# Kernel optimization log

Hardware: AMD Instinct MI355X
Metric: run time of the kernel (lower is better)

Reference implementation:

```python
import jax, jax.numpy as jnp
import numpy as np


def setup_inputs() -> dict:
    key = jax.random.key(0)
    k1, k2, k3 = jax.random.split(key, 3)
    B, L, D = 4, 2056, 1024  # L = K + T = 8 + 2048
    x = jax.random.normal(k1, (B, L, D), dtype=jnp.float32)
    # Linear weights stored as (in_features, out_features); no bias (config.bias=False)
    W_attn = jax.random.normal(k2, (D, 3 * D), dtype=jnp.float32) * 0.02
    W_proj = jax.random.normal(k3, (D, D), dtype=jnp.float32) * 0.02
    return {"x": x, "W_attn": W_attn, "W_proj": W_proj, "n_head": 16, "n_memory": 8}


def reference(x, W_attn, W_proj, n_head, n_memory):
    B, L, C = x.shape
    K = n_memory
    T = L - K
    hd = C // n_head
    scale = 1.0 / np.sqrt(hd).astype(np.float32)

    qkv = x @ W_attn                      # (B, L, 3C)
    q, k, v = jnp.split(qkv, 3, axis=2)
    # (B, H, L, hd)
    q = q.reshape(B, L, n_head, hd).transpose(0, 2, 1, 3)
    k = k.reshape(B, L, n_head, hd).transpose(0, 2, 1, 3)
    v = v.reshape(B, L, n_head, hd).transpose(0, 2, 1, 3)

    att = jnp.einsum("bhqd,bhkd->bhqk", q, k) * scale  # (B, H, L, L)

    # Mask: all-True except the (seq x seq) block which is causal (lower-tri).
    # Memory rows (first K) attend everywhere; seq rows attend to all memory + causal seq.
    mask = jnp.ones((L, L), dtype=bool)
    seq_causal = jnp.tril(jnp.ones((T, T), dtype=bool))
    mask = mask.at[K:, K:].set(seq_causal)

    att = jnp.where(mask[None, None, :, :], att, jnp.float32(-jnp.inf))
    att = jax.nn.softmax(att, axis=-1)

    y = jnp.einsum("bhqk,bhkd->bhqd", att, v)  # (B, H, L, hd)
    y = y.transpose(0, 2, 1, 3).reshape(B, L, C)
    return y @ W_proj
```

## Files before the change

### kernel.cpp

```cpp
#include <hip/hip_runtime.h>
#include <hip/hip_bf16.h>
#include <hip/hip_fp16.h>

typedef _Float16 f16x8 __attribute__((ext_vector_type(8)));
typedef _Float16 f16x4 __attribute__((ext_vector_type(4)));
typedef float f32x4 __attribute__((ext_vector_type(4)));

typedef const __attribute__((address_space(1))) void gvoid_t;
typedef __attribute__((address_space(3))) void svoid_t;

constexpr int Bb = 4, Lq = 2056, Dd = 1024, NH = 16, HD = 64, NMEM = 8;
constexpr int Mtot = Bb * Lq;
constexpr int KEYS = 64;
constexpr int NT = (Lq + KEYS - 1) / KEYS;

__device__ inline float fexp2(float x) {
  float r;
  asm("v_exp_f32 %0, %1" : "=v"(r) : "v"(x));
  return r;
}

__global__ __launch_bounds__(256) void cast_f16(const float* __restrict__ in,
                                                _Float16* __restrict__ out, int n8) {
  int i = blockIdx.x * blockDim.x + threadIdx.x;
  if (i >= n8) return;
  const float4* p = reinterpret_cast<const float4*>(in) + (size_t)i * 2;
  float4 a = p[0], b = p[1];
  f16x8 o;
  o[0] = (_Float16)a.x; o[1] = (_Float16)a.y; o[2] = (_Float16)a.z; o[3] = (_Float16)a.w;
  o[4] = (_Float16)b.x; o[5] = (_Float16)b.y; o[6] = (_Float16)b.z; o[7] = (_Float16)b.w;
  *(reinterpret_cast<f16x8*>(out) + i) = o;
}

__global__ void transpose_cast(const float* __restrict__ in, _Float16* __restrict__ out,
                               int rows, int cols) {
  __shared__ float t[32][33];
  int c0 = blockIdx.x * 32, r0 = blockIdx.y * 32;
  int tx = threadIdx.x, ty = threadIdx.y;
#pragma unroll
  for (int i = 0; i < 4; ++i)
    t[ty + i * 8][tx] = in[(size_t)(r0 + ty + i * 8) * cols + c0 + tx];
  __syncthreads();
#pragma unroll
  for (int i = 0; i < 4; ++i)
    out[(size_t)(c0 + ty + i * 8) * rows + r0 + tx] = (_Float16)t[tx][ty + i * 8];
}

template <int EPI>
__global__ __launch_bounds__(256) void gemm_f16(
    const _Float16* __restrict__ A, const _Float16* __restrict__ Bt,
    int M, int N, int Kd, float* __restrict__ Cf,
    _Float16* __restrict__ qout, _Float16* __restrict__ kout, _Float16* __restrict__ vtout) {
  constexpr int BM = 128, BN = 128, BK = 64;
  __shared__ _Float16 smem[2 * BM * BK];
  const int tid = threadIdx.x;
  const int wid = tid >> 6, lane = tid & 63;
  const int wr = wid >> 1, wc = wid & 1;
  const int l16 = lane & 15, lq = lane >> 4;

  const int gx = gridDim.x;
  const int nwg = gx * gridDim.y;
  const int i0 = blockIdx.y * gx + blockIdx.x;
  const int cpx = nwg >> 3;
  const int logical = (i0 & 7) * cpx + (i0 >> 3);
  const int m0 = (logical / gx) * BM, n0 = (logical % gx) * BN;

  f32x4 acc[4][4];
#pragma unroll
  for (int i = 0; i < 4; ++i)
#pragma unroll
    for (int j = 0; j < 4; ++j) acc[i][j] = (f32x4){0.f, 0.f, 0.f, 0.f};

  const int KT = Kd / BK;
  for (int kt = 0; kt < KT; ++kt) {
    const size_t kbase = (size_t)kt * BK;
#pragma unroll
    for (int c = 0; c < 4; ++c) {
      int q = wid * 256 + c * 64 + lane;
      int r = q >> 3, cc = q & 7;
      int gr = m0 + r; gr = gr < M ? gr : M - 1;
      const _Float16* src = A + (size_t)gr * Kd + kbase + ((cc ^ (r & 7)) << 3);
      __builtin_amdgcn_global_load_lds((gvoid_t*)src,
          (svoid_t*)(smem + (size_t)(wid * 256 + c * 64) * 8), 16, 0, 0);
    }
#pragma unroll
    for (int c = 0; c < 4; ++c) {
      int q = wid * 256 + c * 64 + lane;
      int r = q >> 3, cc = q & 7;
      const _Float16* src = Bt + (size_t)(n0 + r) * Kd + kbase + ((cc ^ (r & 7)) << 3);
      __builtin_amdgcn_global_load_lds((gvoid_t*)src,
          (svoid_t*)(smem + BM * BK + (size_t)(wid * 256 + c * 64) * 8), 16, 0, 0);
    }
    __syncthreads();
#pragma unroll
    for (int kk = 0; kk < 2; ++kk) {
      f16x8 af[4], bfr[4];
#pragma unroll
      for (int i = 0; i < 4; ++i) {
        int r = wr * 64 + i * 16 + l16;
        int off = r * 64 + (((kk * 4 + lq) ^ (r & 7)) << 3);
        af[i] = *(const f16x8*)(smem + off);
      }
#pragma unroll
      for (int j = 0; j < 4; ++j) {
        int r = wc * 64 + j * 16 + l16;
        int off = BM * BK + r * 64 + (((kk * 4 + lq) ^ (r & 7)) << 3);
        bfr[j] = *(const f16x8*)(smem + off);
      }
#pragma unroll
      for (int i = 0; i < 4; ++i)
#pragma unroll
        for (int j = 0; j < 4; ++j)
          acc[i][j] = __builtin_amdgcn_mfma_f32_16x16x32_f16(af[i], bfr[j], acc[i][j], 0, 0, 0);
    }
    __syncthreads();
  }

  if (EPI == 1 && n0 >= 2 * Dd) {
#pragma unroll
    for (int i = 0; i < 4; ++i) {
      int mb = m0 + wr * 64 + i * 16 + lq * 4;
      if (mb >= M) continue;
      int b = mb / Lq, l = mb - b * Lq;
#pragma unroll
      for (int j = 0; j < 4; ++j) {
        int n = n0 + wc * 64 + j * 16 + l16;
        int h = (n >> 6) & 15, d = n & 63;
        if (l + 4 <= Lq) {
          f16x4 pk;
          pk[0] = (_Float16)acc[i][j][0]; pk[1] = (_Float16)acc[i][j][1];
          pk[2] = (_Float16)acc[i][j][2]; pk[3] = (_Float16)acc[i][j][3];
          *(f16x4*)(vtout + ((size_t)(b * NH + h) * HD + d) * Lq + l) = pk;
        } else {
#pragma unroll
          for (int r = 0; r < 4; ++r) {
            int m = mb + r;
            if (m >= M) continue;
            int b2 = m / Lq, l2 = m - b2 * Lq;
            vtout[((size_t)(b2 * NH + h) * HD + d) * Lq + l2] = (_Float16)acc[i][j][r];
          }
        }
      }
    }
  } else {
#pragma unroll
    for (int i = 0; i < 4; ++i) {
#pragma unroll
      for (int r = 0; r < 4; ++r) {
        int m = m0 + wr * 64 + i * 16 + lq * 4 + r;
        if (m >= M) continue;
        if (EPI == 0) {
#pragma unroll
          for (int j = 0; j < 4; ++j) {
            int n = n0 + wc * 64 + j * 16 + l16;
            Cf[(size_t)m * N + n] = acc[i][j][r];
          }
        } else {
          int b = m / Lq, l = m - b * Lq;
#pragma unroll
          for (int j = 0; j < 4; ++j) {
            int n = n0 + wc * 64 + j * 16 + l16;
            int which = n >> 10, h = (n >> 6) & 15, d = n & 63;
            int bh = b * NH + h;
            _Float16 v = (_Float16)acc[i][j][r];
            if (which == 0)
              qout[((size_t)bh * Lq + l) * HD + d] = v;
            else
              kout[((size_t)bh * Lq + l) * HD + d] = v;
          }
        }
      }
    }
  }
}

__global__ __launch_bounds__(256) void attn_f16(const _Float16* __restrict__ qm,
                                                const _Float16* __restrict__ km,
                                                const _Float16* __restrict__ vt,
                                                _Float16* __restrict__ y) {
  __shared__ _Float16 kvs[2][2][KEYS * HD];
  __shared__ _Float16 plds[4][16][40];

  const int i0 = blockIdx.y * (int)gridDim.x + blockIdx.x;
  const int logical = (i0 & 7) * (NT * Bb * NH / 8) + (i0 >> 3);
  const int bh = logical / NT;
  const int qtl = logical % NT;
  const int qt = (qtl == 0) ? 0 : (NT - qtl);

  const int wid = threadIdx.x >> 6, lane = threadIdx.x & 63;
  const int l16 = lane & 15, lq = lane >> 4;
  const int qr0 = qt * 64 + wid * 16;

  const _Float16* qbase = qm + (size_t)bh * Lq * HD;
  const _Float16* kbase = km + (size_t)bh * Lq * HD;
  const _Float16* vbase = vt + (size_t)bh * HD * Lq;

  int qrow = qr0 + l16; if (qrow > Lq - 1) qrow = Lq - 1;
  f16x8 qf0 = *(const f16x8*)(qbase + (size_t)qrow * HD + lq * 8);
  f16x8 qf1 = *(const f16x8*)(qbase + (size_t)qrow * HD + 32 + lq * 8);
  const _Float16 QSC = (_Float16)(0.125f * 1.44269504f);
#pragma unroll
  for (int e = 0; e < 8; ++e) {
    qf0[e] *= QSC;
    qf1[e] *= QSC;
  }

  f16x8 ones;
#pragma unroll
  for (int e = 0; e < 8; ++e) ones[e] = (_Float16)1.0f;

  f32x4 o[4];
#pragma unroll
  for (int dt = 0; dt < 4; ++dt) o[dt] = (f32x4){0.f, 0.f, 0.f, 0.f};
  f32x4 ol = (f32x4){0.f, 0.f, 0.f, 0.f};

  const int ntiles = (qt == 0) ? NT : (qt + 1 < NT ? qt + 1 : NT);

  auto stage = [&](int b, int t) {
    const int j0 = t * KEYS;
#pragma unroll
    for (int c = 0; c < 2; ++c) {
      const int q = (wid * 2 + c) * 64 + lane;
      const int row = q >> 3, cc = q & 7;
      int key = j0 + row; if (key > Lq - 1) key = Lq - 1;
      const _Float16* srcK = kbase + (size_t)key * HD + ((cc ^ (row & 7)) << 3);
      __builtin_amdgcn_global_load_lds((gvoid_t*)srcK,
          (svoid_t*)(&kvs[b][0][(size_t)(wid * 2 + c) * 512]), 16, 0, 0);
      int kc = j0 + ((cc ^ (row & 7)) << 3);
      if (kc + 8 > Lq) kc = Lq - 8;
      const _Float16* srcV = vbase + (size_t)row * Lq + kc;
      __builtin_amdgcn_global_load_lds((gvoid_t*)srcV,
          (svoid_t*)(&kvs[b][1][(size_t)(wid * 2 + c) * 512]), 16, 0, 0);
    }
  };

  stage(0, 0);
  __syncthreads();
  int buf = 0;
  for (int t = 0; t < ntiles; ++t) {
    if (t + 1 < ntiles) stage(buf ^ 1, t + 1);
    const int j0 = t * KEYS;
    const bool fastblk = (t < qt);
    const _Float16* Kl = &kvs[buf][0][0];
    const _Float16* Vl = &kvs[buf][1][0];
#pragma unroll
    for (int ks = 0; ks < 2; ++ks) {
      const int r0 = ks * 32 + l16, r1 = r0 + 16;
      f16x8 ka0 = *(const f16x8*)(Kl + r0 * 64 + ((lq ^ (r0 & 7)) << 3));
      f16x8 kb0 = *(const f16x8*)(Kl + r0 * 64 + (((4 + lq) ^ (r0 & 7)) << 3));
      f16x8 ka1 = *(const f16x8*)(Kl + r1 * 64 + ((lq ^ (r1 & 7)) << 3));
      f16x8 kb1 = *(const f16x8*)(Kl + r1 * 64 + (((4 + lq) ^ (r1 & 7)) << 3));
      f32x4 s0 = (f32x4){0.f, 0.f, 0.f, 0.f};
      f32x4 s1 = (f32x4){0.f, 0.f, 0.f, 0.f};
      __builtin_amdgcn_s_setprio(1);
      s0 = __builtin_amdgcn_mfma_f32_16x16x32_f16(qf0, ka0, s0, 0, 0, 0);
      s0 = __builtin_amdgcn_mfma_f32_16x16x32_f16(qf1, kb0, s0, 0, 0, 0);
      s1 = __builtin_amdgcn_mfma_f32_16x16x32_f16(qf0, ka1, s1, 0, 0, 0);
      s1 = __builtin_amdgcn_mfma_f32_16x16x32_f16(qf1, kb1, s1, 0, 0, 0);
      __builtin_amdgcn_s_setprio(0);

      if (fastblk) {
#pragma unroll
        for (int r = 0; r < 4; ++r) {
          plds[wid][lq * 4 + r][l16] = (_Float16)fexp2(s0[r]);
          plds[wid][lq * 4 + r][l16 + 16] = (_Float16)fexp2(s1[r]);
        }
      } else {
#pragma unroll
        for (int r = 0; r < 4; ++r) {
          int irow = qr0 + lq * 4 + r;
          bool mem = irow < NMEM;
          int c0 = j0 + ks * 32 + l16, c1 = c0 + 16;
          float p0 = (c0 < Lq && (mem || c0 <= irow)) ? fexp2(s0[r]) : 0.f;
          float p1 = (c1 < Lq && (mem || c1 <= irow)) ? fexp2(s1[r]) : 0.f;
          plds[wid][lq * 4 + r][l16] = (_Float16)p0;
          plds[wid][lq * 4 + r][l16 + 16] = (_Float16)p1;
        }
      }
      asm volatile("s_waitcnt lgkmcnt(0)" ::: "memory");
      f16x8 pf = *(const f16x8*)(&plds[wid][l16][lq * 8]);

      __builtin_amdgcn_s_setprio(1);
      ol = __builtin_amdgcn_mfma_f32_16x16x32_f16(pf, ones, ol, 0, 0, 0);
#pragma unroll
      for (int dt = 0; dt < 4; ++dt) {
        int vr = dt * 16 + l16;
        f16x8 vf = *(const f16x8*)(Vl + vr * 64 + ((((ks << 2) | lq) ^ (vr & 7)) << 3));
        o[dt] = __builtin_amdgcn_mfma_f32_16x16x32_f16(pf, vf, o[dt], 0, 0, 0);
      }
      __builtin_amdgcn_s_setprio(0);
    }
    __syncthreads();
    buf ^= 1;
  }

  const int b = bh >> 4, h = bh & 15;
#pragma unroll
  for (int r = 0; r < 4; ++r) {
    int irow = qr0 + lq * 4 + r;
    if (irow >= Lq) continue;
    float inv = 1.0f / ol[r];
#pragma unroll
    for (int dt = 0; dt < 4; ++dt)
      y[((size_t)(b * Lq + irow)) * Dd + h * HD + dt * 16 + l16] = (_Float16)(o[dt][r] * inv);
  }
}

extern "C" void kernel_launch(void* const* d_in, const int* in_sizes, int n_in,
                              void* d_out, int out_size, void* d_ws, size_t ws_size,
                              hipStream_t stream) {
  (void)in_sizes; (void)n_in; (void)out_size; (void)ws_size;
  const float* x = (const float*)d_in[0];
  const float* W_attn = (const float*)d_in[1];
  const float* W_proj = (const float*)d_in[2];
  float* out = (float*)d_out;

  char* w = (char*)d_ws;
  _Float16* xh  = (_Float16*)(w);
  _Float16* wta = (_Float16*)(w + 16842752);
  _Float16* wtp = (_Float16*)(w + 23134208);
  _Float16* qh  = (_Float16*)(w + 25231360);
  _Float16* kh  = (_Float16*)(w + 42074112);
  _Float16* vth = (_Float16*)(w + 58916864);
  _Float16* yh  = xh;

  cast_f16<<<dim3((Mtot * Dd) / 8 / 256), dim3(256), 0, stream>>>(x, xh, (Mtot * Dd) / 8);
  transpose_cast<<<dim3(3 * Dd / 32, Dd / 32), dim3(32, 8), 0, stream>>>(W_attn, wta, Dd, 3 * Dd);
  transpose_cast<<<dim3(Dd / 32, Dd / 32), dim3(32, 8), 0, stream>>>(W_proj, wtp, Dd, Dd);

  gemm_f16<1><<<dim3(3 * Dd / 128, (Mtot + 127) / 128), dim3(256), 0, stream>>>(
      xh, wta, Mtot, 3 * Dd, Dd, nullptr, qh, kh, vth);

  attn_f16<<<dim3(NT, Bb * NH), dim3(256), 0, stream>>>(qh, kh, vth, yh);

  gemm_f16<0><<<dim3(Dd / 128, (Mtot + 127) / 128), dim3(256), 0, stream>>>(
      yh, wtp, Mtot, Dd, Dd, out, nullptr, nullptr, nullptr);
}
```

Baseline: 236.3 us.

## Double query rows per attention block to reuse staged K/V tiles

```diff
diff --git a/kernel.cpp b/kernel.cpp
--- a/kernel.cpp
+++ b/kernel.cpp
@@ -13,6 +13,8 @@
 constexpr int Mtot = Bb * Lq;
 constexpr int KEYS = 64;
 constexpr int NT = (Lq + KEYS - 1) / KEYS;
+constexpr int QB = 128;
+constexpr int NTQ = (Lq + QB - 1) / QB;
 
 __device__ inline float fexp2(float x) {
   float r;
@@ -179,42 +181,49 @@
                                                 const _Float16* __restrict__ vt,
                                                 _Float16* __restrict__ y) {
   __shared__ _Float16 kvs[2][2][KEYS * HD];
-  __shared__ _Float16 plds[4][16][40];
+  __shared__ _Float16 plds[4][2][16][40];
 
   const int i0 = blockIdx.y * (int)gridDim.x + blockIdx.x;
-  const int logical = (i0 & 7) * (NT * Bb * NH / 8) + (i0 >> 3);
-  const int bh = logical / NT;
-  const int qtl = logical % NT;
-  const int qt = (qtl == 0) ? 0 : (NT - qtl);
+  const int logical = (i0 & 7) * (NTQ * Bb * NH / 8) + (i0 >> 3);
+  const int bh = logical / NTQ;
+  const int qtl = logical % NTQ;
+  const int qt = (qtl == 0) ? 0 : (NTQ - qtl);
 
   const int wid = threadIdx.x >> 6, lane = threadIdx.x & 63;
   const int l16 = lane & 15, lq = lane >> 4;
-  const int qr0 = qt * 64 + wid * 16;
+  const int qr0w = qt * QB + wid * 32;
 
   const _Float16* qbase = qm + (size_t)bh * Lq * HD;
   const _Float16* kbase = km + (size_t)bh * Lq * HD;
   const _Float16* vbase = vt + (size_t)bh * HD * Lq;
 
-  int qrow = qr0 + l16; if (qrow > Lq - 1) qrow = Lq - 1;
-  f16x8 qf0 = *(const f16x8*)(qbase + (size_t)qrow * HD + lq * 8);
-  f16x8 qf1 = *(const f16x8*)(qbase + (size_t)qrow * HD + 32 + lq * 8);
   const _Float16 QSC = (_Float16)(0.125f * 1.44269504f);
-#pragma unroll
-  for (int e = 0; e < 8; ++e) {
-    qf0[e] *= QSC;
-    qf1[e] *= QSC;
+  f16x8 qf[2][2];
+#pragma unroll
+  for (int qb = 0; qb < 2; ++qb) {
+    int qrow = qr0w + qb * 16 + l16; if (qrow > Lq - 1) qrow = Lq - 1;
+    qf[qb][0] = *(const f16x8*)(qbase + (size_t)qrow * HD + lq * 8);
+    qf[qb][1] = *(const f16x8*)(qbase + (size_t)qrow * HD + 32 + lq * 8);
+#pragma unroll
+    for (int e = 0; e < 8; ++e) {
+      qf[qb][0][e] *= QSC;
+      qf[qb][1][e] *= QSC;
+    }
   }
 
   f16x8 ones;
 #pragma unroll
   for (int e = 0; e < 8; ++e) ones[e] = (_Float16)1.0f;
 
-  f32x4 o[4];
-#pragma unroll
-  for (int dt = 0; dt < 4; ++dt) o[dt] = (f32x4){0.f, 0.f, 0.f, 0.f};
-  f32x4 ol = (f32x4){0.f, 0.f, 0.f, 0.f};
-
-  const int ntiles = (qt == 0) ? NT : (qt + 1 < NT ? qt + 1 : NT);
+  f32x4 o[2][4];
+#pragma unroll
+  for (int qb = 0; qb < 2; ++qb)
+#pragma unroll
+    for (int dt = 0; dt < 4; ++dt) o[qb][dt] = (f32x4){0.f, 0.f, 0.f, 0.f};
+  f32x4 ol[2] = {(f32x4){0.f, 0.f, 0.f, 0.f}, (f32x4){0.f, 0.f, 0.f, 0.f}};
+
+  const int nt2 = 2 * qt + 2;
+  const int ntiles = (qt == 0) ? NT : (nt2 < NT ? nt2 : NT);
 
   auto stage = [&](int b, int t) {
     const int j0 = t * KEYS;
@@ -240,7 +249,7 @@
   for (int t = 0; t < ntiles; ++t) {
     if (t + 1 < ntiles) stage(buf ^ 1, t + 1);
     const int j0 = t * KEYS;
-    const bool fastblk = (t < qt);
+    const bool fastw = ((t + 1) * KEYS <= qr0w);
     const _Float16* Kl = &kvs[buf][0][0];
     const _Float16* Vl = &kvs[buf][1][0];
 #pragma unroll
@@ -250,43 +259,54 @@
       f16x8 kb0 = *(const f16x8*)(Kl + r0 * 64 + (((4 + lq) ^ (r0 & 7)) << 3));
       f16x8 ka1 = *(const f16x8*)(Kl + r1 * 64 + ((lq ^ (r1 & 7)) << 3));
       f16x8 kb1 = *(const f16x8*)(Kl + r1 * 64 + (((4 + lq) ^ (r1 & 7)) << 3));
-      f32x4 s0 = (f32x4){0.f, 0.f, 0.f, 0.f};
-      f32x4 s1 = (f32x4){0.f, 0.f, 0.f, 0.f};
+      f32x4 s0[2], s1[2];
       __builtin_amdgcn_s_setprio(1);
-      s0 = __builtin_amdgcn_mfma_f32_16x16x32_f16(qf0, ka0, s0, 0, 0, 0);
-      s0 = __builtin_amdgcn_mfma_f32_16x16x32_f16(qf1, kb0, s0, 0, 0, 0);
-      s1 = __builtin_amdgcn_mfma_f32_16x16x32_f16(qf0, ka1, s1, 0, 0, 0);
-      s1 = __builtin_amdgcn_mfma_f32_16x16x32_f16(qf1, kb1, s1, 0, 0, 0);
+#pragma unroll
+      for (int qb = 0; qb < 2; ++qb) {
+        s0[qb] = (f32x4){0.f, 0.f, 0.f, 0.f};
+        s1[qb] = (f32x4){0.f, 0.f, 0.f, 0.f};
+        s0[qb] = __builtin_amdgcn_mfma_f32_16x16x32_f16(qf[qb][0], ka0, s0[qb], 0, 0, 0);
+        s0[qb] = __builtin_amdgcn_mfma_f32_16x16x32_f16(qf[qb][1], kb0, s0[qb], 0, 0, 0);
+        s1[qb] = __builtin_amdgcn_mfma_f32_16x16x32_f16(qf[qb][0], ka1, s1[qb], 0, 0, 0);
+        s1[qb] = __builtin_amdgcn_mfma_f32_16x16x32_f16(qf[qb][1], kb1, s1[qb], 0, 0, 0);
+      }
       __builtin_amdgcn_s_setprio(0);
 
-      if (fastblk) {
-#pragma unroll
-        for (int r = 0; r < 4; ++r) {
-          plds[wid][lq * 4 + r][l16] = (_Float16)fexp2(s0[r]);
-          plds[wid][lq * 4 + r][l16 + 16] = (_Float16)fexp2(s1[r]);
-        }
+      if (fastw) {
+#pragma unroll
+        for (int qb = 0; qb < 2; ++qb)
+#pragma unroll
+          for (int r = 0; r < 4; ++r) {
+            plds[wid][qb][lq * 4 + r][l16] = (_Float16)fexp2(s0[qb][r]);
+            plds[wid][qb][lq * 4 + r][l16 + 16] = (_Float16)fexp2(s1[qb][r]);
+          }
       } else {
 #pragma unroll
-        for (int r = 0; r < 4; ++r) {
-          int irow = qr0 + lq * 4 + r;
-          bool mem = irow < NMEM;
-          int c0 = j0 + ks * 32 + l16, c1 = c0 + 16;
-          float p0 = (c0 < Lq && (mem || c0 <= irow)) ? fexp2(s0[r]) : 0.f;
-          float p1 = (c1 < Lq && (mem || c1 <= irow)) ? fexp2(s1[r]) : 0.f;
-          plds[wid][lq * 4 + r][l16] = (_Float16)p0;
-          plds[wid][lq * 4 + r][l16 + 16] = (_Float16)p1;
-        }
+        for (int qb = 0; qb < 2; ++qb)
+#pragma unroll
+          for (int r = 0; r < 4; ++r) {
+            int irow = qr0w + qb * 16 + lq * 4 + r;
+            bool mem = irow < NMEM;
+            int c0 = j0 + ks * 32 + l16, c1 = c0 + 16;
+            float p0 = (c0 < Lq && (mem || c0 <= irow)) ? fexp2(s0[qb][r]) : 0.f;
+            float p1 = (c1 < Lq && (mem || c1 <= irow)) ? fexp2(s1[qb][r]) : 0.f;
+            plds[wid][qb][lq * 4 + r][l16] = (_Float16)p0;
+            plds[wid][qb][lq * 4 + r][l16 + 16] = (_Float16)p1;
+          }
       }
       asm volatile("s_waitcnt lgkmcnt(0)" ::: "memory");
-      f16x8 pf = *(const f16x8*)(&plds[wid][l16][lq * 8]);
+      f16x8 pf0 = *(const f16x8*)(&plds[wid][0][l16][lq * 8]);
+      f16x8 pf1 = *(const f16x8*)(&plds[wid][1][l16][lq * 8]);
 
       __builtin_amdgcn_s_setprio(1);
-      ol = __builtin_amdgcn_mfma_f32_16x16x32_f16(pf, ones, ol, 0, 0, 0);
+      ol[0] = __builtin_amdgcn_mfma_f32_16x16x32_f16(pf0, ones, ol[0], 0, 0, 0);
+      ol[1] = __builtin_amdgcn_mfma_f32_16x16x32_f16(pf1, ones, ol[1], 0, 0, 0);
 #pragma unroll
       for (int dt = 0; dt < 4; ++dt) {
         int vr = dt * 16 + l16;
         f16x8 vf = *(const f16x8*)(Vl + vr * 64 + ((((ks << 2) | lq) ^ (vr & 7)) << 3));
-        o[dt] = __builtin_amdgcn_mfma_f32_16x16x32_f16(pf, vf, o[dt], 0, 0, 0);
+        o[0][dt] = __builtin_amdgcn_mfma_f32_16x16x32_f16(pf0, vf, o[0][dt], 0, 0, 0);
+        o[1][dt] = __builtin_amdgcn_mfma_f32_16x16x32_f16(pf1, vf, o[1][dt], 0, 0, 0);
       }
       __builtin_amdgcn_s_setprio(0);
     }
@@ -296,14 +316,17 @@
 
   const int b = bh >> 4, h = bh & 15;
 #pragma unroll
-  for (int r = 0; r < 4; ++r) {
-    int irow = qr0 + lq * 4 + r;
-    if (irow >= Lq) continue;
-    float inv = 1.0f / ol[r];
-#pragma unroll
-    for (int dt = 0; dt < 4; ++dt)
-      y[((size_t)(b * Lq + irow)) * Dd + h * HD + dt * 16 + l16] = (_Float16)(o[dt][r] * inv);
-  }
+  for (int qb = 0; qb < 2; ++qb)
+#pragma unroll
+    for (int r = 0; r < 4; ++r) {
+      int irow = qr0w + qb * 16 + lq * 4 + r;
+      if (irow >= Lq) continue;
+      float inv = 1.0f / ol[qb][r];
+#pragma unroll
+      for (int dt = 0; dt < 4; ++dt)
+        y[((size_t)(b * Lq + irow)) * Dd + h * HD + dt * 16 + l16] =
+            (_Float16)(o[qb][dt][r] * inv);
+    }
 }
 
 extern "C" void kernel_launch(void* const* d_in, const int* in_sizes, int n_in,
@@ -331,7 +354,7 @@
   gemm_f16<1><<<dim3(3 * Dd / 128, (Mtot + 127) / 128), dim3(256), 0, stream>>>(
       xh, wta, Mtot, 3 * Dd, Dd, nullptr, qh, kh, vth);
 
-  attn_f16<<<dim3(NT, Bb * NH), dim3(256), 0, stream>>>(qh, kh, vth, yh);
+  attn_f16<<<dim3(NTQ, Bb * NH), dim3(256), 0, stream>>>(qh, kh, vth, yh);
 
   gemm_f16<0><<<dim3(Dd / 128, (Mtot + 127) / 128), dim3(256), 0, stream>>>(
       yh, wtp, Mtot, Dd, Dd, out, nullptr, nullptr, nullptr);
```

Measured after the change: 244.6 us. 1.03x slower.

## Keep attention probabilities in registers by computing transposed QK^T scores

Applied to the files above, without the earlier changes.

```diff
diff --git a/kernel.cpp b/kernel.cpp
--- a/kernel.cpp
+++ b/kernel.cpp
@@ -179,7 +179,6 @@
                                                 const _Float16* __restrict__ vt,
                                                 _Float16* __restrict__ y) {
   __shared__ _Float16 kvs[2][2][KEYS * HD];
-  __shared__ _Float16 plds[4][16][40];
 
   const int i0 = blockIdx.y * (int)gridDim.x + blockIdx.x;
   const int logical = (i0 & 7) * (NT * Bb * NH / 8) + (i0 >> 3);
@@ -204,6 +203,9 @@
     qf0[e] *= QSC;
     qf1[e] *= QSC;
   }
+
+  const int irow = qr0 + l16;
+  const int kmax = (irow < NMEM) ? (Lq - 1) : (irow < Lq - 1 ? irow : Lq - 1);
 
   f16x8 ones;
 #pragma unroll
@@ -240,7 +242,7 @@
   for (int t = 0; t < ntiles; ++t) {
     if (t + 1 < ntiles) stage(buf ^ 1, t + 1);
     const int j0 = t * KEYS;
-    const bool fastblk = (t < qt);
+    const bool fastw = ((t + 1) * KEYS <= qr0);
     const _Float16* Kl = &kvs[buf][0][0];
     const _Float16* Vl = &kvs[buf][1][0];
 #pragma unroll
@@ -253,39 +255,40 @@
       f32x4 s0 = (f32x4){0.f, 0.f, 0.f, 0.f};
       f32x4 s1 = (f32x4){0.f, 0.f, 0.f, 0.f};
       __builtin_amdgcn_s_setprio(1);
-      s0 = __builtin_amdgcn_mfma_f32_16x16x32_f16(qf0, ka0, s0, 0, 0, 0);
-      s0 = __builtin_amdgcn_mfma_f32_16x16x32_f16(qf1, kb0, s0, 0, 0, 0);
-      s1 = __builtin_amdgcn_mfma_f32_16x16x32_f16(qf0, ka1, s1, 0, 0, 0);
-      s1 = __builtin_amdgcn_mfma_f32_16x16x32_f16(qf1, kb1, s1, 0, 0, 0);
+      s0 = __builtin_amdgcn_mfma_f32_16x16x32_f16(ka0, qf0, s0, 0, 0, 0);
+      s0 = __builtin_amdgcn_mfma_f32_16x16x32_f16(kb0, qf1, s0, 0, 0, 0);
+      s1 = __builtin_amdgcn_mfma_f32_16x16x32_f16(ka1, qf0, s1, 0, 0, 0);
+      s1 = __builtin_amdgcn_mfma_f32_16x16x32_f16(kb1, qf1, s1, 0, 0, 0);
       __builtin_amdgcn_s_setprio(0);
 
-      if (fastblk) {
+      f16x8 pf;
+      if (fastw) {
 #pragma unroll
         for (int r = 0; r < 4; ++r) {
-          plds[wid][lq * 4 + r][l16] = (_Float16)fexp2(s0[r]);
-          plds[wid][lq * 4 + r][l16 + 16] = (_Float16)fexp2(s1[r]);
+          pf[r] = (_Float16)fexp2(s0[r]);
+          pf[4 + r] = (_Float16)fexp2(s1[r]);
         }
       } else {
+        const int kb0i = j0 + ks * 32 + lq * 4;
 #pragma unroll
         for (int r = 0; r < 4; ++r) {
-          int irow = qr0 + lq * 4 + r;
-          bool mem = irow < NMEM;
-          int c0 = j0 + ks * 32 + l16, c1 = c0 + 16;
-          float p0 = (c0 < Lq && (mem || c0 <= irow)) ? fexp2(s0[r]) : 0.f;
-          float p1 = (c1 < Lq && (mem || c1 <= irow)) ? fexp2(s1[r]) : 0.f;
-          plds[wid][lq * 4 + r][l16] = (_Float16)p0;
-          plds[wid][lq * 4 + r][l16 + 16] = (_Float16)p1;
+          pf[r] = (kb0i + r <= kmax) ? (_Float16)fexp2(s0[r]) : (_Float16)0.f;
+          pf[4 + r] = (kb0i + 16 + r <= kmax) ? (_Float16)fexp2(s1[r]) : (_Float16)0.f;
         }
       }
-      asm volatile("s_waitcnt lgkmcnt(0)" ::: "memory");
-      f16x8 pf = *(const f16x8*)(&plds[wid][l16][lq * 8]);
 
       __builtin_amdgcn_s_setprio(1);
       ol = __builtin_amdgcn_mfma_f32_16x16x32_f16(pf, ones, ol, 0, 0, 0);
 #pragma unroll
       for (int dt = 0; dt < 4; ++dt) {
-        int vr = dt * 16 + l16;
-        f16x8 vf = *(const f16x8*)(Vl + vr * 64 + ((((ks << 2) | lq) ^ (vr & 7)) << 3));
+        const int vr = dt * 16 + l16;
+        const int g0 = ks * 4 + (lq >> 1);
+        const int wo = (lq & 1) * 4;
+        f16x4 v0 = *(const f16x4*)(Vl + vr * 64 + ((g0 ^ (vr & 7)) << 3) + wo);
+        f16x4 v1 = *(const f16x4*)(Vl + vr * 64 + (((g0 + 2) ^ (vr & 7)) << 3) + wo);
+        f16x8 vf;
+#pragma unroll
+        for (int e = 0; e < 4; ++e) { vf[e] = v0[e]; vf[4 + e] = v1[e]; }
         o[dt] = __builtin_amdgcn_mfma_f32_16x16x32_f16(pf, vf, o[dt], 0, 0, 0);
       }
       __builtin_amdgcn_s_setprio(0);
@@ -297,12 +300,12 @@
   const int b = bh >> 4, h = bh & 15;
 #pragma unroll
   for (int r = 0; r < 4; ++r) {
-    int irow = qr0 + lq * 4 + r;
-    if (irow >= Lq) continue;
+    int orow = qr0 + lq * 4 + r;
+    if (orow >= Lq) continue;
     float inv = 1.0f / ol[r];
 #pragma unroll
     for (int dt = 0; dt < 4; ++dt)
-      y[((size_t)(b * Lq + irow)) * Dd + h * HD + dt * 16 + l16] = (_Float16)(o[dt][r] * inv);
+      y[((size_t)(b * Lq + orow)) * Dd + h * HD + dt * 16 + l16] = (_Float16)(o[dt][r] * inv);
   }
 }
 
```

Measured after the change: 227.4 us (median of 3 runs). 3.8% less time.
